# Performance work log

Measured on AMD Instinct MI355X. Metric: run time of the kernel, lower is better.

The kernel has to match this reference:

```python
import jax, jax.numpy as jnp
import numpy as np

VOCAB, D_IN, D_H, D_OUT = 32000, 512, 1024, 32000
B, S = 64, 512

def setup_inputs() -> dict:
    key = jax.random.key(0)
    ks = jax.random.split(key, 6)
    xav = lambda k, shp: jax.random.uniform(k, shp, jnp.float32, -1.0, 1.0) * np.sqrt(6.0 / (shp[0] + shp[1]))
    return {
        "tokens": jax.random.randint(ks[0], (B, S), 0, VOCAB),
        "h0": jnp.zeros((B, D_H), jnp.float32),
        "embed_table": jax.random.normal(ks[1], (VOCAB, D_IN), jnp.float32),
        "W_ih": xav(ks[2], (D_IN, D_H)),
        "W_hh": xav(ks[3], (D_H, D_H)),
        "bias_hh": jnp.zeros((D_H,), jnp.float32),
        "W_out": xav(ks[4], (D_H, D_OUT)),
        "b_out": jnp.zeros((D_OUT,), jnp.float32),
    }

def reference(tokens, h0, embed_table, W_ih, W_hh, bias_hh, W_out, b_out):
    # embed: [B,S,D_in] -> seq-first [S,B,D_in]
    x = embed_table[tokens].transpose(1, 0, 2)
    # precompute input projection for all timesteps (one big GEMM)
    xw = jnp.einsum("sbi,ih->sbh", x, W_ih) + bias_hh

    def step(h, xw_t):
        h_new = jnp.tanh(xw_t + h @ W_hh)
        return h_new, None

    h_last, _ = jax.lax.scan(step, h0, xw)
    y_pred = h_last @ W_out + b_out  # [B, D_OUT]
    return y_pred
```

## Files before the change

### kernel.cpp

```cpp
#include <hip/hip_runtime.h>

#define D_IN 512
#define D_H 1024
#define D_OUT 32000
#define NB 64
#define NS 512

typedef __attribute__((ext_vector_type(8))) short short8;
typedef __attribute__((ext_vector_type(8))) __bf16 bf16x8;
typedef __attribute__((ext_vector_type(4))) float f32x4;

__device__ __forceinline__ unsigned short f2bf(float f) {
  unsigned int u = __float_as_uint(f);
  u += 0x7fffu + ((u >> 16) & 1u);
  return (unsigned short)(u >> 16);
}
__device__ __forceinline__ float bf2f(unsigned short s) {
  return __uint_as_float(((unsigned int)s) << 16);
}

__device__ __forceinline__ f32x4 mfma_bf16(short8 a, short8 b, f32x4 c) {
  return __builtin_amdgcn_mfma_f32_16x16x32_bf16(
      __builtin_bit_cast(bf16x8, a), __builtin_bit_cast(bf16x8, b), c, 0, 0, 0);
}

union HQ { unsigned long long q[2]; short8 s; };

__global__ __launch_bounds__(256) void rnn_init(const float* __restrict__ h0,
                                                unsigned short* __restrict__ hex,
                                                unsigned int* __restrict__ flags) {
  int idx = blockIdx.x * 256 + threadIdx.x;
  int bg = idx >> 10;
  int k = idx & 1023;
  int g = bg >> 4, bl = bg & 15;
  int c = k >> 5, kk = k & 31;
  float v = h0[idx];
  unsigned short hh = f2bf(v);
  unsigned short hl = f2bf(v - bf2f(hh));
  size_t base = (size_t)(g * 2) * 32768 + (size_t)c * 1024 + bl * 32 + kk;
  hex[base] = hh;
  hex[base + 512] = hl;
  if (blockIdx.x == 0) flags[threadIdx.x] = 0u;
}

__global__ __launch_bounds__(256) void rnn_pack_wih(const float* __restrict__ W_ih,
                                                    unsigned short* __restrict__ bhi,
                                                    unsigned short* __restrict__ blo) {
  int idx = blockIdx.x * 256 + threadIdx.x;
  int j = idx & 7;
  int l = (idx >> 3) & 63;
  int kc = (idx >> 9) & 15;
  int nc = idx >> 13;
  int k = kc * 32 + ((l >> 4) << 3) + j;
  int n = nc * 16 + (l & 15);
  float v = W_ih[(size_t)k * D_H + n];
  unsigned short h = f2bf(v);
  bhi[idx] = h;
  blo[idx] = f2bf(v - bf2f(h));
}

__global__ __launch_bounds__(256) void rnn_stage1(const int* __restrict__ tokens,
                                                  const float* __restrict__ embed,
                                                  const unsigned short* __restrict__ bhi,
                                                  const unsigned short* __restrict__ blo,
                                                  const float* __restrict__ bias,
                                                  float* __restrict__ xw) {
  int bx = blockIdx.x;
  int mt = bx >> 4, nt = bx & 15;
  int tid = threadIdx.x;
  int w = tid >> 6, l = tid & 63;
  int q = l >> 4;

  int m = mt * 64 + w * 16 + (l & 15);
  int b = m & 63, t = m >> 6;
  int tok = tokens[b * NS + t];
  const float* arow = embed + (size_t)tok * D_IN;

  f32x4 acc[4];
#pragma unroll
  for (int i = 0; i < 4; ++i) acc[i] = (f32x4){0.f, 0.f, 0.f, 0.f};

  for (int c = 0; c < 16; ++c) {
    const float* ap = arow + c * 32 + q * 8;
    float4 f0 = *(const float4*)ap;
    float4 f1 = *(const float4*)(ap + 4);
    float fa[8] = {f0.x, f0.y, f0.z, f0.w, f1.x, f1.y, f1.z, f1.w};
    short8 ahi, alo;
#pragma unroll
    for (int j = 0; j < 8; ++j) {
      unsigned short hh = f2bf(fa[j]);
      ahi[j] = (short)hh;
      alo[j] = (short)f2bf(fa[j] - bf2f(hh));
    }
#pragma unroll
    for (int ni = 0; ni < 4; ++ni) {
      int ncg = nt * 4 + ni;
      size_t boff = ((size_t)(ncg * 16 + c) * 64 + l) * 8;
      short8 bh = *(const short8*)(bhi + boff);
      short8 bl_ = *(const short8*)(blo + boff);
      acc[ni] = mfma_bf16(ahi, bh, acc[ni]);
      acc[ni] = mfma_bf16(alo, bh, acc[ni]);
      acc[ni] = mfma_bf16(ahi, bl_, acc[ni]);
    }
  }

#pragma unroll
  for (int ni = 0; ni < 4; ++ni) {
    int col = nt * 64 + ni * 16 + (l & 15);
    float bv = bias[col];
#pragma unroll
    for (int r = 0; r < 4; ++r) {
      int row = mt * 64 + w * 16 + q * 4 + r;
      xw[(size_t)row * D_H + col] = acc[ni][r] + bv;
    }
  }
}

__global__ __launch_bounds__(256, 1) void rnn_recur(const float* __restrict__ xw,
                                                    const float* __restrict__ W_hh,
                                                    unsigned short* __restrict__ hex,
                                                    unsigned int* __restrict__ flags,
                                                    float* __restrict__ h_last) {
  __shared__ short Whi[32768];
  __shared__ short Wlo[32768];
  __shared__ float red[4][16][33];

  const int tid = threadIdx.x;
  const int bx = blockIdx.x;
  const int g = bx >> 5;
  const int jt = bx & 31;
  const int jcol0 = jt * 32;
  const int w = tid >> 6;
  const int l = tid & 63;
  const int q = l >> 4;
  const int b_lane = l & 15;

  for (int v = tid; v < 32768; v += 256) {
    int j = v & 7;
    int ll = (v >> 3) & 63;
    int c = (v >> 9) & 31;
    int s = v >> 14;
    int k = c * 32 + ((ll >> 4) << 3) + j;
    int n = s * 16 + (ll & 15);
    float wv = W_hh[(size_t)k * D_H + jcol0 + n];
    unsigned short hh = f2bf(wv);
    Whi[v] = (short)hh;
    Wlo[v] = (short)f2bf(wv - bf2f(hh));
  }
  __syncthreads();

  unsigned int* flg = flags + g * 32;
  const int fidx = w * 8 + (l & 7);
  const unsigned own = ((jt >> 3) == w) ? (1u << (jt & 7)) : 0u;
  const int loff = b_lane * 64 + q * 16;

  const int be = tid >> 4;
  const int je2 = (tid & 15) * 2;
  const int brow = g * 16 + be;

  char* hexb = (char*)hex;

  float xv0, xv1;
  {
    const float* xwp = xw + ((size_t)0 * 64 + brow) * D_H + jcol0 + je2;
    xv0 = xwp[0];
    xv1 = xwp[1];
  }

  for (int t = 1; t <= NS; ++t) {
    const unsigned target = (unsigned)(t - 1);
    const char* hb = hexb + (size_t)(g * 2 + ((t - 1) & 1)) * 65536;

    f32x4 a00 = {0.f, 0.f, 0.f, 0.f}, a01 = a00, a02 = a00;
    f32x4 a10 = a00, a11 = a00, a12 = a00;

    unsigned done = 0u;
    while (done != 255u) {
      unsigned int fv = __hip_atomic_load(&flg[fidx], __ATOMIC_RELAXED,
                                          __HIP_MEMORY_SCOPE_AGENT);
      unsigned rdy = (((unsigned)__ballot((int)(fv >= target))) & 255u) | own;
      unsigned avail = rdy & ~done;
      if (avail == 0u) continue;
      done |= avail;

      HQ ha_[8], hl_[8];
#pragma unroll
      for (int i = 0; i < 8; ++i) {
        if (avail & (1u << i)) {
          const char* cb = hb + (size_t)(w * 8 + i) * 2048;
          const unsigned long long* ph = (const unsigned long long*)(cb + loff);
          const unsigned long long* pl = (const unsigned long long*)(cb + 1024 + loff);
          ha_[i].q[0] = __hip_atomic_load(ph, __ATOMIC_RELAXED, __HIP_MEMORY_SCOPE_AGENT);
          ha_[i].q[1] = __hip_atomic_load(ph + 1, __ATOMIC_RELAXED, __HIP_MEMORY_SCOPE_AGENT);
          hl_[i].q[0] = __hip_atomic_load(pl, __ATOMIC_RELAXED, __HIP_MEMORY_SCOPE_AGENT);
          hl_[i].q[1] = __hip_atomic_load(pl + 1, __ATOMIC_RELAXED, __HIP_MEMORY_SCOPE_AGENT);
        }
      }
      __builtin_amdgcn_sched_barrier(0);
#pragma unroll
      for (int i = 0; i < 8; ++i) {
        if (avail & (1u << i)) {
          int c = w * 8 + i;
          short8 bh0 = *(const short8*)(Whi + c * 512 + l * 8);
          short8 bl0 = *(const short8*)(Wlo + c * 512 + l * 8);
          short8 bh1 = *(const short8*)(Whi + 16384 + c * 512 + l * 8);
          short8 bl1 = *(const short8*)(Wlo + 16384 + c * 512 + l * 8);
          a00 = mfma_bf16(ha_[i].s, bh0, a00);
          a01 = mfma_bf16(hl_[i].s, bh0, a01);
          a02 = mfma_bf16(ha_[i].s, bl0, a02);
          a10 = mfma_bf16(ha_[i].s, bh1, a10);
          a11 = mfma_bf16(hl_[i].s, bh1, a11);
          a12 = mfma_bf16(ha_[i].s, bl1, a12);
        }
      }
    }

    f32x4 s0 = a00 + a01 + a02;
    f32x4 s1 = a10 + a11 + a12;
#pragma unroll
    for (int r = 0; r < 4; ++r) {
      red[w][q * 4 + r][b_lane] = s0[r];
      red[w][q * 4 + r][16 + b_lane] = s1[r];
    }
    __syncthreads();

    float z0 = red[0][be][je2] + red[1][be][je2] + red[2][be][je2] +
               red[3][be][je2] + xv0;
    float z1 = red[0][be][je2 + 1] + red[1][be][je2 + 1] + red[2][be][je2 + 1] +
               red[3][be][je2 + 1] + xv1;
    float hv0 = tanhf(z0);
    float hv1 = tanhf(z1);
    unsigned short h0h = f2bf(hv0), h1h = f2bf(hv1);
    unsigned short h0l = f2bf(hv0 - bf2f(h0h)), h1l = f2bf(hv1 - bf2f(h1h));
    char* wb = hexb + (size_t)(g * 2 + (t & 1)) * 65536 + (size_t)jt * 2048;
    unsigned int* dhi = (unsigned int*)(wb + be * 64 + je2 * 2);
    unsigned int* dlo = (unsigned int*)(wb + 1024 + be * 64 + je2 * 2);
    unsigned int phi = (unsigned int)h0h | ((unsigned int)h1h << 16);
    unsigned int plo = (unsigned int)h0l | ((unsigned int)h1l << 16);
    __hip_atomic_store(dhi, phi, __ATOMIC_RELAXED, __HIP_MEMORY_SCOPE_AGENT);
    __hip_atomic_store(dlo, plo, __ATOMIC_RELAXED, __HIP_MEMORY_SCOPE_AGENT);
    if (t == NS) {
      h_last[(size_t)brow * 1024 + jcol0 + je2] = hv0;
      h_last[(size_t)brow * 1024 + jcol0 + je2 + 1] = hv1;
    }

    asm volatile("s_waitcnt vmcnt(0)" ::: "memory");
    if (t < NS) {
      const float* xwp = xw + ((size_t)t * 64 + brow) * D_H + jcol0 + je2;
      xv0 = xwp[0];
      xv1 = xwp[1];
    }
    __syncthreads();
    if (tid == 0)
      __hip_atomic_store(&flg[jt], (unsigned int)t, __ATOMIC_RELAXED,
                         __HIP_MEMORY_SCOPE_AGENT);
  }
}

__global__ __launch_bounds__(256, 2) void rnn_out(const float* __restrict__ h_last,
                                                  const float* __restrict__ W_out,
                                                  const float* __restrict__ b_out,
                                                  float* __restrict__ out) {
  __shared__ float smem[16384];
  int tid = threadIdx.x;
  int jl = tid & 127;
  int kh = tid >> 7;
  int j = blockIdx.x * 128 + jl;

  float acc[64];
#pragma unroll
  for (int b = 0; b < 64; ++b) acc[b] = 0.f;

  for (int kc = 0; kc < 4; ++kc) {
    __syncthreads();
    for (int v = tid; v < 16384; v += 256) {
      int kh2 = v >> 13;
      int b = (v >> 7) & 63;
      int kk = v & 127;
      smem[v] = h_last[(size_t)b * 1024 + kh2 * 512 + kc * 128 + kk];
    }
    __syncthreads();
    int kbase = kh * 512 + kc * 128;
    for (int kkc = 0; kkc < 16; ++kkc) {
      float wreg[8];
#pragma unroll
      for (int i = 0; i < 8; ++i)
        wreg[i] = W_out[(size_t)(kbase + kkc * 8 + i) * D_OUT + j];
#pragma unroll
      for (int b = 0; b < 64; ++b) {
        const float* hp = &smem[kh * 8192 + b * 128 + kkc * 8];
#pragma unroll
        for (int i = 0; i < 8; ++i) acc[b] += hp[i] * wreg[i];
      }
    }
  }
  __syncthreads();
  if (kh == 1) {
#pragma unroll
    for (int b = 0; b < 64; ++b) smem[jl * 65 + b] = acc[b];
  }
  __syncthreads();
  if (kh == 0) {
    float bo = b_out[j];
#pragma unroll
    for (int b = 0; b < 64; ++b)
      out[(size_t)b * D_OUT + j] = acc[b] + smem[jl * 65 + b] + bo;
  }
}

extern "C" void kernel_launch(void* const* d_in, const int* in_sizes, int n_in,
                              void* d_out, int out_size, void* d_ws, size_t ws_size,
                              hipStream_t stream) {
  const int* tokens = (const int*)d_in[0];
  const float* h0 = (const float*)d_in[1];
  const float* embed = (const float*)d_in[2];
  const float* W_ih = (const float*)d_in[3];
  const float* W_hh = (const float*)d_in[4];
  const float* bias_hh = (const float*)d_in[5];
  const float* W_out = (const float*)d_in[6];
  const float* b_out = (const float*)d_in[7];
  float* out = (float*)d_out;

  char* ws = (char*)d_ws;
  float* xw = (float*)(ws);
  unsigned short* wih_hi = (unsigned short*)(ws + 134217728);
  unsigned short* wih_lo = (unsigned short*)(ws + 135266304);
  unsigned short* hex = (unsigned short*)(ws + 136314880);
  unsigned int* flags = (unsigned int*)(ws + 136839168);
  float* h_last = (float*)(ws + 136840192);

  rnn_init<<<256, 256, 0, stream>>>(h0, hex, flags);
  rnn_pack_wih<<<2048, 256, 0, stream>>>(W_ih, wih_hi, wih_lo);
  rnn_stage1<<<8192, 256, 0, stream>>>(tokens, embed, wih_hi, wih_lo, bias_hh, xw);
  rnn_recur<<<128, 256, 0, stream>>>(xw, W_hh, hex, flags, h_last);
  rnn_out<<<250, 256, 0, stream>>>(h_last, W_out, b_out, out);
}
```

Measured before the change: 2.968 ms.

## Replace flag-based step sync with tagged hidden-state words polled directly

Removes the per-block progress flags and instead embeds a parity tag in bit 30 of each fp32 hidden value, so consumers poll the data itself with cache-bypassing loads and proceed once every word carries the expected tag. Each block also reuses its own tile from shared memory instead of reloading it from global memory. This drops the flag-store round trip and the vmcnt wait before the flag, which shortens the critical path of each of the 512 recurrent steps. In exchange the exchange buffer holds fp32 instead of bf16 hi/lo pairs, so more bytes move per step, and the hi/lo split is recomputed by every consumer. Clearing bit 30 of the hidden value is safe only because tanh output has magnitude at most 1.

Result: slower. 3.175 ms (+7.0%).

```diff
diff --git a/kernel.cpp b/kernel.cpp
--- a/kernel.cpp
+++ b/kernel.cpp
@@ -9,6 +9,7 @@
 typedef __attribute__((ext_vector_type(8))) short short8;
 typedef __attribute__((ext_vector_type(8))) __bf16 bf16x8;
 typedef __attribute__((ext_vector_type(4))) float f32x4;
+typedef __attribute__((ext_vector_type(4))) unsigned int u32x4;
 
 __device__ __forceinline__ unsigned short f2bf(float f) {
   unsigned int u = __float_as_uint(f);
@@ -24,23 +25,33 @@
       __builtin_bit_cast(bf16x8, a), __builtin_bit_cast(bf16x8, b), c, 0, 0, 0);
 }
 
-union HQ { unsigned long long q[2]; short8 s; };
+__device__ __forceinline__ u32x4 ld16_cc(const void* p) {
+  u32x4 v;
+  asm volatile("global_load_dwordx4 %0, %1, off sc0 sc1"
+               : "=v"(v) : "v"(p) : "memory");
+  return v;
+}
+__device__ __forceinline__ void st8_cc(void* p, unsigned long long v) {
+  asm volatile("global_store_dwordx2 %0, %1, off sc0 sc1"
+               :: "v"(p), "v"(v) : "memory");
+}
 
 __global__ __launch_bounds__(256) void rnn_init(const float* __restrict__ h0,
-                                                unsigned short* __restrict__ hex,
-                                                unsigned int* __restrict__ flags) {
+                                                unsigned int* __restrict__ hexw) {
   int idx = blockIdx.x * 256 + threadIdx.x;
-  int bg = idx >> 10;
-  int k = idx & 1023;
-  int g = bg >> 4, bl = bg & 15;
-  int c = k >> 5, kk = k & 31;
-  float v = h0[idx];
-  unsigned short hh = f2bf(v);
-  unsigned short hl = f2bf(v - bf2f(hh));
-  size_t base = (size_t)(g * 2) * 32768 + (size_t)c * 1024 + bl * 32 + kk;
-  hex[base] = hh;
-  hex[base + 512] = hl;
-  if (blockIdx.x == 0) flags[threadIdx.x] = 0u;
+  int kk = idx & 31;
+  int b = (idx >> 5) & 15;
+  int c = (idx >> 9) & 31;
+  int buf = (idx >> 14) & 1;
+  int g = idx >> 15;
+  unsigned w;
+  if (buf == 0) {
+    float v = h0[(size_t)(g * 16 + b) * 1024 + c * 32 + kk];
+    w = __float_as_uint(v) & 0xBFFFFFFFu;
+  } else {
+    w = 0x40000000u;
+  }
+  hexw[idx] = w;
 }
 
 __global__ __launch_bounds__(256) void rnn_pack_wih(const float* __restrict__ W_ih,
@@ -116,14 +127,36 @@
   }
 }
 
+#define CONSUME_W(Wa, cc)                                              \
+  {                                                                    \
+    short8 ah_, al_;                                                   \
+    _Pragma("unroll")                                                  \
+    for (int m_ = 0; m_ < 8; ++m_) {                                   \
+      float v_ = __uint_as_float(Wa[m_] & 0xBFFFFFFFu);                \
+      unsigned short hh_ = f2bf(v_);                                   \
+      ah_[m_] = (short)hh_;                                            \
+      al_[m_] = (short)f2bf(v_ - bf2f(hh_));                           \
+    }                                                                  \
+    short8 bh0_ = *(const short8*)(Whi + (cc) * 512 + l * 8);          \
+    short8 bl0_ = *(const short8*)(Wlo + (cc) * 512 + l * 8);          \
+    short8 bh1_ = *(const short8*)(Whi + 16384 + (cc) * 512 + l * 8);  \
+    short8 bl1_ = *(const short8*)(Wlo + 16384 + (cc) * 512 + l * 8);  \
+    a00 = mfma_bf16(ah_, bh0_, a00);                                   \
+    a01 = mfma_bf16(al_, bh0_, a01);                                   \
+    a02 = mfma_bf16(ah_, bl0_, a02);                                   \
+    a10 = mfma_bf16(ah_, bh1_, a10);                                   \
+    a11 = mfma_bf16(al_, bh1_, a11);                                   \
+    a12 = mfma_bf16(ah_, bl1_, a12);                                   \
+  }
+
 __global__ __launch_bounds__(256, 1) void rnn_recur(const float* __restrict__ xw,
                                                     const float* __restrict__ W_hh,
-                                                    unsigned short* __restrict__ hex,
-                                                    unsigned int* __restrict__ flags,
+                                                    unsigned int* __restrict__ hexw,
                                                     float* __restrict__ h_last) {
   __shared__ short Whi[32768];
   __shared__ short Wlo[32768];
   __shared__ float red[4][16][33];
+  __shared__ float ownF[16 * 33];
 
   const int tid = threadIdx.x;
   const int bx = blockIdx.x;
@@ -139,80 +172,81 @@
     int j = v & 7;
     int ll = (v >> 3) & 63;
     int c = (v >> 9) & 31;
-    int s = v >> 14;
+    int s2 = v >> 14;
     int k = c * 32 + ((ll >> 4) << 3) + j;
-    int n = s * 16 + (ll & 15);
+    int n = s2 * 16 + (ll & 15);
     float wv = W_hh[(size_t)k * D_H + jcol0 + n];
     unsigned short hh = f2bf(wv);
     Whi[v] = (short)hh;
     Wlo[v] = (short)f2bf(wv - bf2f(hh));
   }
-  __syncthreads();
-
-  unsigned int* flg = flags + g * 32;
-  const int fidx = w * 8 + (l & 7);
-  const unsigned own = ((jt >> 3) == w) ? (1u << (jt & 7)) : 0u;
-  const int loff = b_lane * 64 + q * 16;
+
+  const bool ownw = ((jt >> 3) == w);
+  const unsigned ownbit = 1u << (jt & 7);
+  const int loff = b_lane * 128 + q * 32;
 
   const int be = tid >> 4;
   const int je2 = (tid & 15) * 2;
   const int brow = g * 16 + be;
 
-  char* hexb = (char*)hex;
+  char* hexb = (char*)hexw;
 
   float xv0, xv1;
   {
-    const float* xwp = xw + ((size_t)0 * 64 + brow) * D_H + jcol0 + je2;
+    const float* xwp = xw + (size_t)brow * D_H + jcol0 + je2;
     xv0 = xwp[0];
     xv1 = xwp[1];
   }
+  __syncthreads();
 
   for (int t = 1; t <= NS; ++t) {
-    const unsigned target = (unsigned)(t - 1);
+    const unsigned expw = (unsigned)(((t - 1) >> 1) & 1) << 30;
     const char* hb = hexb + (size_t)(g * 2 + ((t - 1) & 1)) * 65536;
 
     f32x4 a00 = {0.f, 0.f, 0.f, 0.f}, a01 = a00, a02 = a00;
     f32x4 a10 = a00, a11 = a00, a12 = a00;
 
-    unsigned done = 0u;
-    while (done != 255u) {
-      unsigned int fv = __hip_atomic_load(&flg[fidx], __ATOMIC_RELAXED,
-                                          __HIP_MEMORY_SCOPE_AGENT);
-      unsigned rdy = (((unsigned)__ballot((int)(fv >= target))) & 255u) | own;
-      unsigned avail = rdy & ~done;
-      if (avail == 0u) continue;
-      done |= avail;
-
-      HQ ha_[8], hl_[8];
+    const bool useown = ownw && (t > 1);
+    unsigned need = useown ? (255u & ~ownbit) : 255u;
+    bool first = true;
+    u32x4 GA[8], GB[8];
+
+    while (need) {
+      const unsigned m0 = need;
 #pragma unroll
       for (int i = 0; i < 8; ++i) {
-        if (avail & (1u << i)) {
-          const char* cb = hb + (size_t)(w * 8 + i) * 2048;
-          const unsigned long long* ph = (const unsigned long long*)(cb + loff);
-          const unsigned long long* pl = (const unsigned long long*)(cb + 1024 + loff);
-          ha_[i].q[0] = __hip_atomic_load(ph, __ATOMIC_RELAXED, __HIP_MEMORY_SCOPE_AGENT);
-          ha_[i].q[1] = __hip_atomic_load(ph + 1, __ATOMIC_RELAXED, __HIP_MEMORY_SCOPE_AGENT);
-          hl_[i].q[0] = __hip_atomic_load(pl, __ATOMIC_RELAXED, __HIP_MEMORY_SCOPE_AGENT);
-          hl_[i].q[1] = __hip_atomic_load(pl + 1, __ATOMIC_RELAXED, __HIP_MEMORY_SCOPE_AGENT);
+        if (m0 & (1u << i)) {
+          const char* cb = hb + (size_t)(w * 8 + i) * 2048 + loff;
+          GA[i] = ld16_cc(cb);
+          GB[i] = ld16_cc(cb + 16);
         }
       }
+      if (first && useown) {
+        unsigned Wo[8];
+#pragma unroll
+        for (int m_ = 0; m_ < 8; ++m_)
+          Wo[m_] = __float_as_uint(ownF[b_lane * 33 + q * 8 + m_]);
+        CONSUME_W(Wo, jt);
+      }
+      asm volatile("s_waitcnt vmcnt(0)" ::: "memory");
       __builtin_amdgcn_sched_barrier(0);
+
 #pragma unroll
       for (int i = 0; i < 8; ++i) {
-        if (avail & (1u << i)) {
-          int c = w * 8 + i;
-          short8 bh0 = *(const short8*)(Whi + c * 512 + l * 8);
-          short8 bl0 = *(const short8*)(Wlo + c * 512 + l * 8);
-          short8 bh1 = *(const short8*)(Whi + 16384 + c * 512 + l * 8);
-          short8 bl1 = *(const short8*)(Wlo + 16384 + c * 512 + l * 8);
-          a00 = mfma_bf16(ha_[i].s, bh0, a00);
-          a01 = mfma_bf16(hl_[i].s, bh0, a01);
-          a02 = mfma_bf16(ha_[i].s, bl0, a02);
-          a10 = mfma_bf16(ha_[i].s, bh1, a10);
-          a11 = mfma_bf16(hl_[i].s, bh1, a11);
-          a12 = mfma_bf16(ha_[i].s, bl1, a12);
+        if (m0 & (1u << i)) {
+          unsigned bad = (GA[i].x ^ expw) | (GA[i].y ^ expw) |
+                         (GA[i].z ^ expw) | (GA[i].w ^ expw) |
+                         (GB[i].x ^ expw) | (GB[i].y ^ expw) |
+                         (GB[i].z ^ expw) | (GB[i].w ^ expw);
+          if (__all((int)((bad & 0x40000000u) == 0u))) {
+            need &= ~(1u << i);
+            unsigned W_[8] = {GA[i].x, GA[i].y, GA[i].z, GA[i].w,
+                              GB[i].x, GB[i].y, GB[i].z, GB[i].w};
+            CONSUME_W(W_, w * 8 + i);
+          }
         }
       }
+      first = false;
     }
 
     f32x4 s0 = a00 + a01 + a02;
@@ -230,30 +264,24 @@
                red[3][be][je2 + 1] + xv1;
     float hv0 = tanhf(z0);
     float hv1 = tanhf(z1);
-    unsigned short h0h = f2bf(hv0), h1h = f2bf(hv1);
-    unsigned short h0l = f2bf(hv0 - bf2f(h0h)), h1l = f2bf(hv1 - bf2f(h1h));
-    char* wb = hexb + (size_t)(g * 2 + (t & 1)) * 65536 + (size_t)jt * 2048;
-    unsigned int* dhi = (unsigned int*)(wb + be * 64 + je2 * 2);
-    unsigned int* dlo = (unsigned int*)(wb + 1024 + be * 64 + je2 * 2);
-    unsigned int phi = (unsigned int)h0h | ((unsigned int)h1h << 16);
-    unsigned int plo = (unsigned int)h0l | ((unsigned int)h1l << 16);
-    __hip_atomic_store(dhi, phi, __ATOMIC_RELAXED, __HIP_MEMORY_SCOPE_AGENT);
-    __hip_atomic_store(dlo, plo, __ATOMIC_RELAXED, __HIP_MEMORY_SCOPE_AGENT);
+    ownF[be * 33 + je2] = hv0;
+    ownF[be * 33 + je2 + 1] = hv1;
+    const unsigned tagw = (unsigned)((t >> 1) & 1) << 30;
+    unsigned w0 = (__float_as_uint(hv0) & 0xBFFFFFFFu) | tagw;
+    unsigned w1 = (__float_as_uint(hv1) & 0xBFFFFFFFu) | tagw;
+    char* wb = hexb + (size_t)(g * 2 + (t & 1)) * 65536 + (size_t)jt * 2048 +
+               be * 128 + je2 * 4;
+    st8_cc(wb, (unsigned long long)w0 | ((unsigned long long)w1 << 32));
+
     if (t == NS) {
       h_last[(size_t)brow * 1024 + jcol0 + je2] = hv0;
       h_last[(size_t)brow * 1024 + jcol0 + je2 + 1] = hv1;
-    }
-
-    asm volatile("s_waitcnt vmcnt(0)" ::: "memory");
-    if (t < NS) {
+    } else {
       const float* xwp = xw + ((size_t)t * 64 + brow) * D_H + jcol0 + je2;
       xv0 = xwp[0];
       xv1 = xwp[1];
     }
     __syncthreads();
-    if (tid == 0)
-      __hip_atomic_store(&flg[jt], (unsigned int)t, __ATOMIC_RELAXED,
-                         __HIP_MEMORY_SCOPE_AGENT);
   }
 }
 
@@ -325,13 +353,12 @@
   float* xw = (float*)(ws);
   unsigned short* wih_hi = (unsigned short*)(ws + 134217728);
   unsigned short* wih_lo = (unsigned short*)(ws + 135266304);
-  unsigned short* hex = (unsigned short*)(ws + 136314880);
-  unsigned int* flags = (unsigned int*)(ws + 136839168);
-  float* h_last = (float*)(ws + 136840192);
-
-  rnn_init<<<256, 256, 0, stream>>>(h0, hex, flags);
+  unsigned int* hexw = (unsigned int*)(ws + 136314880);
+  float* h_last = (float*)(ws + 136839168);
+
+  rnn_init<<<512, 256, 0, stream>>>(h0, hexw);
   rnn_pack_wih<<<2048, 256, 0, stream>>>(W_ih, wih_hi, wih_lo);
   rnn_stage1<<<8192, 256, 0, stream>>>(tokens, embed, wih_hi, wih_lo, bias_hh, xw);
-  rnn_recur<<<128, 256, 0, stream>>>(xw, W_hh, hex, flags, h_last);
+  rnn_recur<<<128, 256, 0, stream>>>(xw, W_hh, hexw, h_last);
   rnn_out<<<250, 256, 0, stream>>>(h_last, W_out, b_out, out);
 }
```
